# Optimization experiments

Hardware: AMD Instinct MI355X
Metric: run time of the kernel (lower is better)

Reference implementation:

```python
import jax, jax.numpy as jnp
import numpy as np

D_MODEL = 256
NUM_HEADS = 8
WINDOW = 7
B, H, W = 2, 56, 56


def setup_inputs() -> dict:
    key = jax.random.key(0)
    ks = jax.random.split(key, 9)
    s = D_MODEL ** -0.5
    return {
        "x": jax.random.normal(ks[0], (B, D_MODEL, H, W), jnp.float32),
        "wq": jax.random.normal(ks[1], (D_MODEL, D_MODEL), jnp.float32) * s,
        "bq": jnp.zeros((D_MODEL,), jnp.float32),
        "wk": jax.random.normal(ks[2], (D_MODEL, D_MODEL), jnp.float32) * s,
        "bk": jnp.zeros((D_MODEL,), jnp.float32),
        "wv": jax.random.normal(ks[3], (D_MODEL, D_MODEL), jnp.float32) * s,
        "bv": jnp.zeros((D_MODEL,), jnp.float32),
        "wo": jax.random.normal(ks[4], (D_MODEL, D_MODEL), jnp.float32) * s,
        "bo": jnp.zeros((D_MODEL,), jnp.float32),
    }


def _proj(x, w, b):
    # 1x1 conv == channel matmul. x: [B,C,H,W], w: [Cout,Cin], b: [Cout]
    return jnp.einsum('oc,bchw->bohw', w, x) + b[None, :, None, None]


def _windows(t, ws):
    # t: [B,h,d,H,W] -> [B,h,d,H,W,ws*ws], zero-padded sliding windows.
    # Row-major (i*ws + j) flattening matches torch unfold(3).unfold(4).view(...,-1).
    pad = ws // 2
    Hh, Ww = t.shape[-2], t.shape[-1]
    tp = jnp.pad(t, ((0, 0), (0, 0), (0, 0), (pad, pad), (pad, pad)))
    return jnp.stack([tp[..., i:i + Hh, j:j + Ww]
                      for i in range(ws) for j in range(ws)], axis=-1)


def reference(x, wq, bq, wk, bk, wv, bv, wo, bo):
    Bt, C, Hh, Ww = x.shape
    hd = C // NUM_HEADS
    scale = hd ** -0.5
    q = _proj(x, wq, bq).reshape(Bt, NUM_HEADS, hd, Hh, Ww)
    k = _proj(x, wk, bk).reshape(Bt, NUM_HEADS, hd, Hh, Ww)
    v = _proj(x, wv, bv).reshape(Bt, NUM_HEADS, hd, Hh, Ww)
    kw = _windows(k, WINDOW)  # [B,h,d,H,W,ws^2]
    vw = _windows(v, WINDOW)
    attn = jnp.einsum('bhdxy,bhdxyw->bhxyw', q, kw) * scale
    attn = jax.nn.softmax(attn, axis=-1)
    out = jnp.einsum('bhxyw,bhdxyw->bhdxy', attn, vw).reshape(Bt, C, Hh, Ww)
    return _proj(out, wo, bo)
```

## Files before the change

kernel.cpp:

```cpp
#include <hip/hip_runtime.h>
#include <cstdint>

#define NHEAD 8
#define HD 32
#define DM 256
#define HH 56
#define WWID 56
#define HW 3136
#define NB 2
#define SCALE 0.17677669529663687f

#if __has_builtin(__builtin_amdgcn_exp2f)
#define QSCALE 0.25503488f
#define EXPW(x) __builtin_amdgcn_exp2f(x)
#else
#define QSCALE SCALE
#define EXPW(x) __expf(x)
#endif

typedef _Float16 f16;
typedef __attribute__((ext_vector_type(2))) _Float16 f16x2;
typedef __attribute__((ext_vector_type(8))) _Float16 f16x8;
typedef __attribute__((ext_vector_type(4))) float floatx4;

union U16 { uint4 u; f16x2 h2[4]; f16 h[8]; };

#define GLD16(g, l) __builtin_amdgcn_global_load_lds( \
    (__attribute__((address_space(1))) void*)(g),     \
    (__attribute__((address_space(3))) void*)(l), 16, 0, 0)

#if __has_builtin(__builtin_amdgcn_update_dpp)
__device__ __forceinline__ float quad_sum(float s) {
    float t1 = __int_as_float(__builtin_amdgcn_update_dpp(
        0, __float_as_int(s), 0xB1, 0xF, 0xF, true));
    s += t1;
    float t2 = __int_as_float(__builtin_amdgcn_update_dpp(
        0, __float_as_int(s), 0x4E, 0xF, 0xF, true));
    return s + t2;
}
#else
__device__ __forceinline__ float quad_sum(float s) {
    s += __shfl_xor(s, 1);
    s += __shfl_xor(s, 2);
    return s;
}
#endif

__global__ __launch_bounds__(256) void prep(
    const float* __restrict__ x,
    const float* __restrict__ wq, const float* __restrict__ wk,
    const float* __restrict__ wv, const float* __restrict__ wo,
    f16* __restrict__ xT, f16* __restrict__ wcat, f16* __restrict__ wob)
{
    const int bid = blockIdx.x;
    const int t = threadIdx.x;
    if (bid < 1568) {
        __shared__ float tile[32][33];
        const int b = bid / 784, r = bid - 784 * b;
        const int ct = r / 98;
        const int p0 = (r - ct * 98) * 32, c0 = ct * 32;
        const int tx = t & 31, ty = t >> 5;
        const float* xb = x + (size_t)b * DM * HW;
        #pragma unroll
        for (int i = 0; i < 4; ++i)
            tile[ty + i * 8][tx] = xb[(size_t)(c0 + ty + i * 8) * HW + p0 + tx];
        __syncthreads();
        f16* xo = xT + (size_t)b * HW * DM;
        #pragma unroll
        for (int i = 0; i < 4; ++i)
            xo[(size_t)(p0 + ty + i * 8) * DM + c0 + tx] =
                (f16)tile[tx][ty + i * 8];
    } else {
        const int gid = (bid - 1568) * 256 + t;
        const int idx4 = gid << 2;
        const int sel = idx4 >> 16;
        const int off = idx4 & 65535;
        const float* src = sel == 0 ? wq : (sel == 1 ? wk : (sel == 2 ? wv : wo));
        f16* dst = sel < 3 ? (wcat + (sel << 16) + off) : (wob + off);
        float4 f = *(const float4*)&src[off];
        union { ushort4 u; f16 h[4]; } pk;
        pk.h[0] = (f16)f.x; pk.h[1] = (f16)f.y;
        pk.h[2] = (f16)f.z; pk.h[3] = (f16)f.w;
        *(ushort4*)dst = pk.u;
    }
}

template<int MODE>
__global__ __launch_bounds__(256) void gemm_mfma(
    const f16* __restrict__ A,
    const f16* __restrict__ Bm,
    const float* __restrict__ b0, const float* __restrict__ b1,
    const float* __restrict__ b2,
    void* __restrict__ o0, void* __restrict__ o1, void* __restrict__ o2)
{
    const int bb = blockIdx.z;
    const int n0 = blockIdx.x * 64;
    const int m0 = blockIdx.y * 128;
    const f16* Bb = Bm + (size_t)bb * HW * DM + (size_t)n0 * DM;

    __shared__ __align__(16) f16 As[128][32];
    __shared__ __align__(16) f16 Bs[64][32];

    const int t = threadIdx.x;
    const int wave = t >> 6, lane = t & 63;
    const int quad = lane >> 4, l16 = lane & 15;
    const int mw = (wave & 1) * 64, nw = (wave >> 1) * 32;

    floatx4 acc[4][2] = {};

    const int sr = t >> 2;
    const int sq = (t & 3) << 3;
    const f16* gA = A + (size_t)(m0 + sr) * DM + sq;
    const f16* gB = Bb + (size_t)sr * DM + sq;
    f16* lA  = &As[sr][sq];
    f16* lA2 = &As[sr + 64][sq];
    f16* lB  = &Bs[sr][sq];

    for (int k0 = 0; k0 < DM; k0 += 32) {
        GLD16(gA + k0, lA);
        GLD16(gA + 64 * DM + k0, lA2);
        GLD16(gB + k0, lB);
        __syncthreads();
        f16x8 af[4], bf[2];
        #pragma unroll
        for (int mt = 0; mt < 4; ++mt)
            af[mt] = *(const f16x8*)&As[mw + mt * 16 + l16][quad * 8];
        #pragma unroll
        for (int nt = 0; nt < 2; ++nt)
            bf[nt] = *(const f16x8*)&Bs[nw + nt * 16 + l16][quad * 8];
        #pragma unroll
        for (int mt = 0; mt < 4; ++mt)
            #pragma unroll
            for (int nt = 0; nt < 2; ++nt)
                acc[mt][nt] = __builtin_amdgcn_mfma_f32_16x16x32_f16(
                    af[mt], bf[nt], acc[mt][nt], 0, 0, 0);
        __syncthreads();
    }

    if (MODE == 0) {
        #pragma unroll
        for (int mt = 0; mt < 4; ++mt) {
            const int gm = m0 + mw + mt * 16 + quad * 4;
            const int proj = gm >> 8;
            const int c = gm & 255;
            const int h = c >> 5, d0 = c & 31;
            const float* bptr = proj == 0 ? b0 : (proj == 1 ? b1 : b2);
            f16* op = (f16*)(proj == 0 ? o0 : (proj == 1 ? o1 : o2));
            const float sc = proj == 0 ? QSCALE : 1.0f;
            const size_t base = ((size_t)(bb * NHEAD + h) * HW) * HD + d0;
            float bias[4] = {bptr[c], bptr[c + 1], bptr[c + 2], bptr[c + 3]};
            #pragma unroll
            for (int nt = 0; nt < 2; ++nt) {
                const int p = n0 + nw + nt * 16 + l16;
                union { ushort4 u; f16 h[4]; } pk;
                #pragma unroll
                for (int r = 0; r < 4; ++r)
                    pk.h[r] = (f16)((acc[mt][nt][r] + bias[r]) * sc);
                *(ushort4*)&op[base + (size_t)p * HD] = pk.u;
            }
        }
    } else {
        float* yo = (float*)o0;
        #pragma unroll
        for (int mt = 0; mt < 4; ++mt) {
            const int gc = m0 + mw + mt * 16 + quad * 4;
            #pragma unroll
            for (int r = 0; r < 4; ++r) {
                const float bias = b0[gc + r];
                #pragma unroll
                for (int nt = 0; nt < 2; ++nt) {
                    const int p = n0 + nw + nt * 16 + l16;
                    yo[(size_t)(bb * DM + gc + r) * HW + p] = acc[mt][nt][r] + bias;
                }
            }
        }
    }
}

#define HROWS 8
#define HPOS  (HROWS * WWID)
#define HPP   (HPOS + 6)

__global__ __launch_bounds__(448) void attn_win(
    const f16* __restrict__ q,
    const f16* __restrict__ k,
    const f16* __restrict__ v,
    f16* __restrict__ out)
{
    __shared__ uint4 kh[HPP * 4];
    __shared__ uint4 vh[HPP * 4];

    const int t = threadIdx.x;
    const int tile = blockIdx.x;
    const int h = blockIdx.y, b = blockIdx.z;
    const int y0 = tile * 2;
    const size_t base = (size_t)(b * NHEAD + h) * HW * HD;
    const f16* kp = k + base;
    const f16* vp = v + base;

    #pragma unroll
    for (int it = 0; it < 4; ++it) {
        const int u = t + it * 448;
        const int pos = u >> 2, ch = u & 3;
        const int hr = pos / WWID;
        const int gx = pos - hr * WWID;
        const int gy = y0 - 3 + hr;
        uint4 kv = make_uint4(0, 0, 0, 0), vv = make_uint4(0, 0, 0, 0);
        if ((unsigned)gy < HH) {
            const size_t g = (size_t)(gy * WWID + gx) * HD + (ch << 3);
            kv = *(const uint4*)&kp[g];
            vv = *(const uint4*)&vp[g];
        }
        kh[u + 12] = kv;
        vh[u + 12] = vv;
    }
    if (t < 48) {
        const int ps = t % 6;
        const int fi = (ps < 3 ? ps * 4 : (HPOS + ps) * 4) + ((t / 6) & 3);
        const uint4 z = make_uint4(0, 0, 0, 0);
        if (t < 24) kh[fi] = z; else vh[fi] = z;
    }
    __syncthreads();

    const int pl = t >> 2;
    const int ch = t & 3;
    const int lx = pl >= WWID ? pl - WWID : pl;
    const int p = y0 * WWID + pl;

    U16 qu;
    qu.u = *(const uint4*)(q + base + (size_t)p * HD + (ch << 3));

    const uint4* kb4 = kh + t;
    const uint4* vb4 = vh + t;

    float wm[7];
    #pragma unroll
    for (int j = 0; j < 7; ++j)
        wm[j] = ((unsigned)(lx + j - 3) < WWID) ? 1.0f : 0.0f;
    const int nin = (lx < 3 ? 3 - lx : 0) + (lx > 52 ? lx - 52 : 0);

    float of[8] = {};
    float sum = (float)(7 * nin);
    for (int i = 0; i < 7; ++i) {
        #pragma unroll
        for (int j = 0; j < 7; ++j) {
            const int off4 = (i * WWID + j) << 2;
            U16 ku; ku.u = kb4[off4];
            float s;
            s = __builtin_amdgcn_fdot2(ku.h2[0], qu.h2[0], 0.0f, false);
            s = __builtin_amdgcn_fdot2(ku.h2[1], qu.h2[1], s, false);
            s = __builtin_amdgcn_fdot2(ku.h2[2], qu.h2[2], s, false);
            s = __builtin_amdgcn_fdot2(ku.h2[3], qu.h2[3], s, false);
            s = quad_sum(s);
            const float e = EXPW(s);
            const float wt = e * wm[j];
            sum += wt;
            U16 vu; vu.u = vb4[off4];
            of[0] = fmaf((float)vu.h[0], wt, of[0]);
            of[1] = fmaf((float)vu.h[1], wt, of[1]);
            of[2] = fmaf((float)vu.h[2], wt, of[2]);
            of[3] = fmaf((float)vu.h[3], wt, of[3]);
            of[4] = fmaf((float)vu.h[4], wt, of[4]);
            of[5] = fmaf((float)vu.h[5], wt, of[5]);
            of[6] = fmaf((float)vu.h[6], wt, of[6]);
            of[7] = fmaf((float)vu.h[7], wt, of[7]);
        }
    }

#if __has_builtin(__builtin_amdgcn_rcpf)
    const float inv = __builtin_amdgcn_rcpf(sum);
#else
    const float inv = 1.0f / sum;
#endif
    f16* op = out + ((size_t)b * HW + p) * DM + h * HD + (ch << 3);
    U16 ou;
    #pragma unroll
    for (int j = 0; j < 8; ++j)
        ou.h[j] = (f16)(of[j] * inv);
    *(uint4*)op = ou.u;
}

extern "C" void kernel_launch(void* const* d_in, const int* in_sizes, int n_in,
                              void* d_out, int out_size, void* d_ws, size_t ws_size,
                              hipStream_t stream) {
    const float* x  = (const float*)d_in[0];
    const float* wq = (const float*)d_in[1];
    const float* bq = (const float*)d_in[2];
    const float* wk = (const float*)d_in[3];
    const float* bk = (const float*)d_in[4];
    const float* wv = (const float*)d_in[5];
    const float* bv = (const float*)d_in[6];
    const float* wo = (const float*)d_in[7];
    const float* bo = (const float*)d_in[8];
    float* out = (float*)d_out;

    const size_t NPC = (size_t)NB * HW * DM;
    f16* xT    = (f16*)d_ws;
    f16* wcat  = xT + NPC;
    f16* wob   = wcat + 768 * 256;
    f16* qb    = wob + 256 * 256;
    f16* kb    = qb + NPC;
    f16* vb    = kb + NPC;
    f16* attnT = vb + NPC;

    prep<<<1824, 256, 0, stream>>>(x, wq, wk, wv, wo, xT, wcat, wob);
    gemm_mfma<0><<<dim3(HW / 64, 6, NB), 256, 0, stream>>>(
        wcat, xT, bq, bk, bv, qb, kb, vb);
    attn_win<<<dim3(28, NHEAD, NB), 448, 0, stream>>>(qb, kb, vb, attnT);
    gemm_mfma<1><<<dim3(HW / 64, 2, NB), 256, 0, stream>>>(
        wob, attnT, bo, bo, bo, out, out, out);
}
```

Before: 106.6 us.

## Double-buffer GEMM LDS tiles and compute two horizontal pixels per attention thread

The MFMA GEMM now double-buffers its LDS tiles. It issues the next k-slice's async global-to-LDS loads before computing on the current one, using explicit vmcnt waits and raw barriers. The windowed attention kernel now handles two adjacent pixels per thread group with half the threads. Each K/V row of 8 window columns is read from shared memory once and reused for both queries' 7-wide windows, cutting LDS traffic. The costs are more registers per thread, fewer waves per block, and hand-managed waitcnt synchronisation that could be fragile.

```diff
diff --git a/kernel.cpp b/kernel.cpp
--- a/kernel.cpp
+++ b/kernel.cpp
@@ -45,6 +45,14 @@
     return s;
 }
 #endif
+
+__device__ __forceinline__ float dot8(const U16& a, const U16& b) {
+    float s = __builtin_amdgcn_fdot2(a.h2[0], b.h2[0], 0.0f, false);
+    s = __builtin_amdgcn_fdot2(a.h2[1], b.h2[1], s, false);
+    s = __builtin_amdgcn_fdot2(a.h2[2], b.h2[2], s, false);
+    s = __builtin_amdgcn_fdot2(a.h2[3], b.h2[3], s, false);
+    return s;
+}
 
 __global__ __launch_bounds__(256) void prep(
     const float* __restrict__ x,
@@ -98,8 +106,8 @@
     const int m0 = blockIdx.y * 128;
     const f16* Bb = Bm + (size_t)bb * HW * DM + (size_t)n0 * DM;
 
-    __shared__ __align__(16) f16 As[128][32];
-    __shared__ __align__(16) f16 Bs[64][32];
+    __shared__ __align__(16) f16 As[2][128][32];
+    __shared__ __align__(16) f16 Bs[2][64][32];
 
     const int t = threadIdx.x;
     const int wave = t >> 6, lane = t & 63;
@@ -112,29 +120,44 @@
     const int sq = (t & 3) << 3;
     const f16* gA = A + (size_t)(m0 + sr) * DM + sq;
     const f16* gB = Bb + (size_t)sr * DM + sq;
-    f16* lA  = &As[sr][sq];
-    f16* lA2 = &As[sr + 64][sq];
-    f16* lB  = &Bs[sr][sq];
-
-    for (int k0 = 0; k0 < DM; k0 += 32) {
-        GLD16(gA + k0, lA);
-        GLD16(gA + 64 * DM + k0, lA2);
-        GLD16(gB + k0, lB);
-        __syncthreads();
+    f16* lA[2]  = { &As[0][sr][sq],      &As[1][sr][sq]      };
+    f16* lA2[2] = { &As[0][sr + 64][sq], &As[1][sr + 64][sq] };
+    f16* lB[2]  = { &Bs[0][sr][sq],      &Bs[1][sr][sq]      };
+
+    GLD16(gA, lA[0]);
+    GLD16(gA + 64 * DM, lA2[0]);
+    GLD16(gB, lB[0]);
+
+    #pragma unroll
+    for (int kk = 0; kk < 8; ++kk) {
+        const int cur = kk & 1, nxt = cur ^ 1;
+        if (kk < 7) {
+            const int ko = (kk + 1) * 32;
+            GLD16(gA + ko, lA[nxt]);
+            GLD16(gA + 64 * DM + ko, lA2[nxt]);
+            GLD16(gB + ko, lB[nxt]);
+            asm volatile("s_waitcnt vmcnt(3)" ::: "memory");
+        } else {
+            asm volatile("s_waitcnt vmcnt(0)" ::: "memory");
+        }
+        __builtin_amdgcn_s_barrier();
+        __builtin_amdgcn_sched_barrier(0);
         f16x8 af[4], bf[2];
         #pragma unroll
         for (int mt = 0; mt < 4; ++mt)
-            af[mt] = *(const f16x8*)&As[mw + mt * 16 + l16][quad * 8];
+            af[mt] = *(const f16x8*)&As[cur][mw + mt * 16 + l16][quad * 8];
         #pragma unroll
         for (int nt = 0; nt < 2; ++nt)
-            bf[nt] = *(const f16x8*)&Bs[nw + nt * 16 + l16][quad * 8];
+            bf[nt] = *(const f16x8*)&Bs[cur][nw + nt * 16 + l16][quad * 8];
         #pragma unroll
         for (int mt = 0; mt < 4; ++mt)
             #pragma unroll
             for (int nt = 0; nt < 2; ++nt)
                 acc[mt][nt] = __builtin_amdgcn_mfma_f32_16x16x32_f16(
                     af[mt], bf[nt], acc[mt][nt], 0, 0, 0);
-        __syncthreads();
+        asm volatile("s_waitcnt lgkmcnt(0)" ::: "memory");
+        __builtin_amdgcn_sched_barrier(0);
+        __builtin_amdgcn_s_barrier();
     }
 
     if (MODE == 0) {
@@ -181,7 +204,7 @@
 #define HPOS  (HROWS * WWID)
 #define HPP   (HPOS + 6)
 
-__global__ __launch_bounds__(448) void attn_win(
+__global__ __launch_bounds__(224) void attn_win(
     const f16* __restrict__ q,
     const f16* __restrict__ k,
     const f16* __restrict__ v,
@@ -199,8 +222,8 @@
     const f16* vp = v + base;
 
     #pragma unroll
-    for (int it = 0; it < 4; ++it) {
-        const int u = t + it * 448;
+    for (int it = 0; it < 8; ++it) {
+        const int u = t + it * 224;
         const int pos = u >> 2, ch = u & 3;
         const int hr = pos / WWID;
         const int gx = pos - hr * WWID;
@@ -222,62 +245,76 @@
     }
     __syncthreads();
 
-    const int pl = t >> 2;
+    const int g  = t >> 2;
     const int ch = t & 3;
-    const int lx = pl >= WWID ? pl - WWID : pl;
-    const int p = y0 * WWID + pl;
-
-    U16 qu;
-    qu.u = *(const uint4*)(q + base + (size_t)p * HD + (ch << 3));
-
-    const uint4* kb4 = kh + t;
-    const uint4* vb4 = vh + t;
-
-    float wm[7];
+    const int ry = g >= 28 ? 1 : 0;
+    const int px = g - ry * 28;
+    const int x0 = px * 2;
+    const int plA = ry * WWID + x0;
+    const int pA = y0 * WWID + plA;
+    const int tA = plA * 4 + ch;
+
+    U16 qa, qb;
+    qa.u = *(const uint4*)(q + base + (size_t)pA * HD + (ch << 3));
+    qb.u = *(const uint4*)(q + base + (size_t)(pA + 1) * HD + (ch << 3));
+
+    const uint4* kb4 = kh + tA;
+    const uint4* vb4 = vh + tA;
+
+    float inr[8];
+    float cA = 0.f, cB = 0.f;
     #pragma unroll
-    for (int j = 0; j < 7; ++j)
-        wm[j] = ((unsigned)(lx + j - 3) < WWID) ? 1.0f : 0.0f;
-    const int nin = (lx < 3 ? 3 - lx : 0) + (lx > 52 ? lx - 52 : 0);
-
-    float of[8] = {};
-    float sum = (float)(7 * nin);
+    for (int c = 0; c < 8; ++c) {
+        inr[c] = ((unsigned)(x0 + c - 3) < WWID) ? 1.0f : 0.0f;
+        if (c < 7) cA += inr[c];
+        if (c > 0) cB += inr[c];
+    }
+    float ofA[8] = {}, ofB[8] = {};
+    float sumA = 7.0f * (7.0f - cA);
+    float sumB = 7.0f * (7.0f - cB);
+
     for (int i = 0; i < 7; ++i) {
         #pragma unroll
-        for (int j = 0; j < 7; ++j) {
-            const int off4 = (i * WWID + j) << 2;
+        for (int c = 0; c < 8; ++c) {
+            const int off4 = (i * WWID + c) << 2;
             U16 ku; ku.u = kb4[off4];
-            float s;
-            s = __builtin_amdgcn_fdot2(ku.h2[0], qu.h2[0], 0.0f, false);
-            s = __builtin_amdgcn_fdot2(ku.h2[1], qu.h2[1], s, false);
-            s = __builtin_amdgcn_fdot2(ku.h2[2], qu.h2[2], s, false);
-            s = __builtin_amdgcn_fdot2(ku.h2[3], qu.h2[3], s, false);
-            s = quad_sum(s);
-            const float e = EXPW(s);
-            const float wt = e * wm[j];
-            sum += wt;
             U16 vu; vu.u = vb4[off4];
-            of[0] = fmaf((float)vu.h[0], wt, of[0]);
-            of[1] = fmaf((float)vu.h[1], wt, of[1]);
-            of[2] = fmaf((float)vu.h[2], wt, of[2]);
-            of[3] = fmaf((float)vu.h[3], wt, of[3]);
-            of[4] = fmaf((float)vu.h[4], wt, of[4]);
-            of[5] = fmaf((float)vu.h[5], wt, of[5]);
-            of[6] = fmaf((float)vu.h[6], wt, of[6]);
-            of[7] = fmaf((float)vu.h[7], wt, of[7]);
+            if (c < 7) {
+                float s = quad_sum(dot8(ku, qa));
+                const float w = EXPW(s) * inr[c];
+                sumA += w;
+                #pragma unroll
+                for (int n = 0; n < 8; ++n)
+                    ofA[n] = fmaf((float)vu.h[n], w, ofA[n]);
+            }
+            if (c > 0) {
+                float s = quad_sum(dot8(ku, qb));
+                const float w = EXPW(s) * inr[c];
+                sumB += w;
+                #pragma unroll
+                for (int n = 0; n < 8; ++n)
+                    ofB[n] = fmaf((float)vu.h[n], w, ofB[n]);
+            }
         }
     }
 
 #if __has_builtin(__builtin_amdgcn_rcpf)
-    const float inv = __builtin_amdgcn_rcpf(sum);
+    const float invA = __builtin_amdgcn_rcpf(sumA);
+    const float invB = __builtin_amdgcn_rcpf(sumB);
 #else
-    const float inv = 1.0f / sum;
+    const float invA = 1.0f / sumA;
+    const float invB = 1.0f / sumB;
 #endif
-    f16* op = out + ((size_t)b * HW + p) * DM + h * HD + (ch << 3);
-    U16 ou;
+    f16* opA = out + ((size_t)b * HW + pA) * DM + h * HD + (ch << 3);
+    f16* opB = opA + DM;
+    U16 oa, ob;
     #pragma unroll
-    for (int j = 0; j < 8; ++j)
-        ou.h[j] = (f16)(of[j] * inv);
-    *(uint4*)op = ou.u;
+    for (int n = 0; n < 8; ++n) {
+        oa.h[n] = (f16)(ofA[n] * invA);
+        ob.h[n] = (f16)(ofB[n] * invB);
+    }
+    *(uint4*)opA = oa.u;
+    *(uint4*)opB = ob.u;
 }
 
 extern "C" void kernel_launch(void* const* d_in, const int* in_sizes, int n_in,
@@ -306,7 +343,7 @@
     prep<<<1824, 256, 0, stream>>>(x, wq, wk, wv, wo, xT, wcat, wob);
     gemm_mfma<0><<<dim3(HW / 64, 6, NB), 256, 0, stream>>>(
         wcat, xT, bq, bk, bv, qb, kb, vb);
-    attn_win<<<dim3(28, NHEAD, NB), 448, 0, stream>>>(qb, kb, vb, attnT);
+    attn_win<<<dim3(28, NHEAD, NB), 224, 0, stream>>>(qb, kb, vb, attnT);
     gemm_mfma<1><<<dim3(HW / 64, 2, NB), 256, 0, stream>>>(
         wob, attnT, bo, bo, bo, out, out, out);
 }
```

New measurement: 105.5 us. About the same (-1.0%).
